# Optimization experiments

Hardware: AMD Instinct MI355X
Metric: run time of the kernel (lower is better)

The kernel has to match this reference:

```python
import jax, jax.numpy as jnp
import numpy as np

B, C, H, W = 1, 512, 64, 64
HEADS, DIM_HEAD = 8, 64
GROUPS = 32
EPS = 1e-5
SCALE = DIM_HEAD ** -0.5


def setup_inputs() -> dict:
    key = jax.random.key(0)
    ks = jax.random.split(key, 8)
    inner = HEADS * DIM_HEAD  # 512
    s = 0.02
    return {
        "hidden_states": jax.random.normal(ks[0], (B, C, H, W), jnp.float32),
        "gn_gamma": jnp.ones((C,), jnp.float32),
        "gn_beta": jnp.zeros((C,), jnp.float32),
        "wq": jax.random.normal(ks[1], (inner, C), jnp.float32) * s,
        "wk": jax.random.normal(ks[2], (inner, C), jnp.float32) * s,
        "wv": jax.random.normal(ks[3], (inner, C), jnp.float32) * s,
        "wo": jax.random.normal(ks[4], (C, inner), jnp.float32) * s,
        "bo": jnp.zeros((C,), jnp.float32),
    }


def _group_norm(x, gamma, beta):
    # x: [B, C, H, W]; normalize within channel groups over (C//G, H, W)
    b, c, h, w = x.shape
    xg = x.reshape(b, GROUPS, c // GROUPS, h, w)
    mean = xg.mean(axis=(2, 3, 4), keepdims=True)
    var = xg.var(axis=(2, 3, 4), keepdims=True)
    xg = (xg - mean) * jax.lax.rsqrt(var + EPS)
    x = xg.reshape(b, c, h, w)
    return x * gamma[None, :, None, None] + beta[None, :, None, None]


def reference(hidden_states, gn_gamma, gn_beta, wq, wk, wv, wo, bo):
    residual = hidden_states
    x = _group_norm(hidden_states, gn_gamma, gn_beta)
    b, c, h, w = x.shape
    n = h * w
    x = x.reshape(b, c, n).transpose(0, 2, 1)  # [B, N, C]

    # torch Linear: y = x @ W^T (bias=False for q/k/v)
    q = (x @ wq.T).reshape(b, n, HEADS, DIM_HEAD).transpose(0, 2, 1, 3)  # [B,H,N,D]
    k = (x @ wk.T).reshape(b, n, HEADS, DIM_HEAD).transpose(0, 2, 1, 3)
    v = (x @ wv.T).reshape(b, n, HEADS, DIM_HEAD).transpose(0, 2, 1, 3)

    scores = jnp.einsum("bhqd,bhkd->bhqk", q, k) * SCALE  # [B,H,N,N]
    probs = jax.nn.softmax(scores, axis=-1)
    out = jnp.einsum("bhqk,bhkd->bhqd", probs, v)  # [B,H,N,D]

    out = out.transpose(0, 2, 1, 3).reshape(b, n, HEADS * DIM_HEAD)  # [B,N,inner]
    out = out @ wo.T + bo  # [B,N,C]
    out = out.transpose(0, 2, 1).reshape(b, c, h, w)
    return out + residual
```

## Files before the change

kernel.cpp:

```cpp
#include <hip/hip_runtime.h>

#define N_TOK 4096
#define C_DIM 512
#define NH    8
#define EPS   1e-5f
#define NSPLIT 4
#define THR   11.0f

typedef __attribute__((ext_vector_type(8))) __bf16 bf16x8;
typedef __attribute__((ext_vector_type(4))) float  f32x4;
using u16 = unsigned short;
using u32 = unsigned int;

#define MFMA16 __builtin_amdgcn_mfma_f32_16x16x32_bf16

__device__ __forceinline__ u16 f2bf(float f){
  u32 x = __builtin_bit_cast(u32, f);
  x += 0x7fffu + ((x>>16)&1u);
  return (u16)(x>>16);
}
__device__ __forceinline__ float bf2f(u16 v){
  return __builtin_bit_cast(float, (u32)v<<16);
}
__device__ __forceinline__ float exp2a(float x){
  float r; asm("v_exp_f32 %0, %1" : "=v"(r) : "v"(x)); return r;
}
__device__ __forceinline__ u32 cvtpk(float lo, float hi){
  u32 r; asm("v_cvt_pk_bf16_f32 %0, %1, %2" : "=v"(r) : "v"(lo), "v"(hi)); return r;
}
__device__ __forceinline__ float max3a(float a, float b, float c){
  float r; asm("v_max3_f32 %0, %1, %2, %3" : "=v"(r) : "v"(a), "v"(b), "v"(c)); return r;
}
__device__ __forceinline__ void dma16(const void* src, void* lds){
  __builtin_amdgcn_global_load_lds(
      (const __attribute__((address_space(1))) u32*)src,
      (__attribute__((address_space(3))) u32*)lds, 16, 0, 0);
}

__global__ __launch_bounds__(256) void k_pre(const float* __restrict__ s0,
      const float* __restrict__ s1, const float* __restrict__ s2,
      const float* __restrict__ s3, u16* __restrict__ d0, u16* __restrict__ d1,
      u16* __restrict__ d2, u16* __restrict__ d3,
      const float* __restrict__ x, float* __restrict__ pstat,
      u16* __restrict__ xbf){
  __shared__ float rs[4], rss[4];
  int b = blockIdx.x;
  if (b < 1024){
    int m = b >> 8;
    int i = (b & 255)*256 + threadIdx.x;
    const float* s = m==0?s0 : m==1?s1 : m==2?s2 : s3;
    u16*         d = m==0?d0 : m==1?d1 : m==2?d2 : d3;
    float4 v = ((const float4*)s)[i];
    ushort4 o; o.x=f2bf(v.x); o.y=f2bf(v.y); o.z=f2bf(v.z); o.w=f2bf(v.w);
    ((ushort4*)d)[i] = o;
    return;
  }
  int gb = b - 1024;
  int g = gb>>3, p = gb&7, t = threadIdx.x;
  const float4* gx4 = (const float4*)(x + (size_t)g*16*N_TOK) + (size_t)p*2048;
  ushort4* xb4 = (ushort4*)xbf + (size_t)g*16384 + (size_t)p*2048;
  float s=0.f, ss=0.f;
  #pragma unroll
  for (int k=0;k<8;k++){
    float4 v = gx4[t + k*256];
    s  += v.x+v.y+v.z+v.w;
    ss += v.x*v.x+v.y*v.y+v.z*v.z+v.w*v.w;
    ushort4 o; o.x=f2bf(v.x); o.y=f2bf(v.y); o.z=f2bf(v.z); o.w=f2bf(v.w);
    xb4[t + k*256] = o;
  }
  for (int m=1;m<64;m<<=1){ s += __shfl_xor(s,m); ss += __shfl_xor(ss,m); }
  int w=t>>6, lane=t&63;
  if (lane==0){ rs[w]=s; rss[w]=ss; }
  __syncthreads();
  if (t==0){
    pstat[(g*8+p)*2  ] = rs[0]+rs[1]+rs[2]+rs[3];
    pstat[(g*8+p)*2+1] = rss[0]+rss[1]+rss[2]+rss[3];
  }
}

__global__ __launch_bounds__(256) void k_gn_apply(const u16* __restrict__ xbf,
      const float* __restrict__ pstat, const float* __restrict__ gamma,
      const float* __restrict__ beta, u16* __restrict__ X){
  int g = blockIdx.x, c0 = g*16;
  int n = blockIdx.y*256 + threadIdx.x;
  float S=0.f, SS=0.f;
  #pragma unroll
  for (int p=0;p<8;p++){ S += pstat[(g*8+p)*2]; SS += pstat[(g*8+p)*2+1]; }
  float mean = S*(1.f/65536.f);
  float rstd = rsqrtf(SS*(1.f/65536.f) - mean*mean + EPS);
  u16 ov[16];
  #pragma unroll
  for (int c=0;c<16;c++){
    float gm = gamma[c0+c]*rstd;
    float be = beta[c0+c] - mean*gm;
    float v  = bf2f(xbf[(size_t)(c0+c)*N_TOK + n])*gm + be;
    ov[c] = f2bf(v);
  }
  uint4* dst = (uint4*)&X[(size_t)n*C_DIM + c0];
  dst[0] = *(uint4*)&ov[0];
  dst[1] = *(uint4*)&ov[8];
}

__device__ __forceinline__ void gemm_core64(const u16* A, const u16* B,
      int m0, int n0, char* LDS, f32x4 (&acc)[4][2]){
  int t = threadIdx.x, w = t>>6, l = t&63, lr = l&15, li = l>>4;
  int wr = w>>1, wc = w&1;
  char* As = LDS;
  char* Bs = LDS + 32768;
  const char* Ac = (const char*)A + (size_t)m0*1024;
  const char* Bc = (const char*)B + (size_t)n0*1024;
  int rswz = (lr&7)<<4;

  int rowA[4], segA[4], rowB[2], segB[2];
  #pragma unroll
  for (int k=0;k<4;k++){ int s=t+k*256; rowA[k]=s>>3; segA[k]=s&7; }
  #pragma unroll
  for (int k=0;k<2;k++){ int s=t+k*256; rowB[k]=s>>3; segB[k]=s&7; }

  #define STAGE(it, bb) { int koff=(it)*128;                                   \
    _Pragma("unroll")                                                          \
    for (int k=0;k<4;k++){                                                     \
      int ys = (segA[k]*16) ^ ((rowA[k]&7)<<4);                                \
      dma16(Ac + (size_t)rowA[k]*1024 + koff + ys,                             \
            As + (bb)*16384 + w*1024 + k*4096);                                \
    }                                                                          \
    _Pragma("unroll")                                                          \
    for (int k=0;k<2;k++){                                                     \
      int ys = (segB[k]*16) ^ ((rowB[k]&7)<<4);                                \
      dma16(Bc + (size_t)rowB[k]*1024 + koff + ys,                             \
            Bs + (bb)*8192 + w*1024 + k*4096);                                 \
    } }

  STAGE(0, 0);
  __syncthreads();

  int buf = 0;
  for (int it=0; it<8; it++){
    if (it < 7){ STAGE(it+1, buf^1); }
    char* Ab = As + buf*16384;
    char* Bb = Bs + buf*8192;
    #pragma unroll
    for (int ks=0; ks<2; ks++){
      bf16x8 af[4], bfr[2];
      #pragma unroll
      for (int i=0;i<4;i++){
        int ra = wr*64 + i*16 + lr;
        af[i]  = *(const bf16x8*)(Ab + ra*128 + ((li*16 + ks*64) ^ rswz));
      }
      #pragma unroll
      for (int j=0;j<2;j++){
        int rb = wc*32 + j*16 + lr;
        bfr[j] = *(const bf16x8*)(Bb + rb*128 + ((li*16 + ks*64) ^ rswz));
      }
      __builtin_amdgcn_s_setprio(1);
      #pragma unroll
      for (int i=0;i<4;i++){
        #pragma unroll
        for (int j=0;j<2;j++){
          acc[i][j] = MFMA16(af[i], bfr[j], acc[i][j], 0,0,0);
        }
      }
      __builtin_amdgcn_s_setprio(0);
    }
    __syncthreads();
    buf ^= 1;
  }
  #undef STAGE
}

__global__ __launch_bounds__(256,3) void k_qkv2(const u16* __restrict__ X,
      const u16* __restrict__ wq, const u16* __restrict__ wk,
      const u16* __restrict__ wv, u16* __restrict__ Qo, u16* __restrict__ Ko,
      u16* __restrict__ Vto){
  __shared__ char LDS[49152];
  int b = blockIdx.x;
  const u16 *A, *B; u16* Cp; int ldc, m0, n0; float sc = 1.f; bool vperm = false;
  if (b < 256){        A=X;  B=wq; Cp=Qo;  ldc=512;  m0=(b>>3)*128; n0=(b&7)*64;
                       sc = 0.125f*1.44269504f; }
  else if (b < 512){ int r=b-256; A=X;  B=wk; Cp=Ko;  ldc=512;  m0=(r>>3)*128; n0=(r&7)*64; }
  else             { int r=b-512; A=wv; B=X;  Cp=Vto; ldc=4096; m0=(r>>6)*128; n0=(r&63)*64;
                     vperm = true; }

  f32x4 acc[4][2] = {};
  gemm_core64(A, B, m0, n0, LDS, acc);

  int t = threadIdx.x, w = t>>6, l = t&63, lr = l&15, li = l>>4;
  int wr = w>>1, wc = w&1;
  #pragma unroll
  for (int i=0;i<4;i++){
    #pragma unroll
    for (int rr=0;rr<4;rr++){
      int mm = m0 + wr*64 + i*16 + li*4 + rr;
      #pragma unroll
      for (int j=0;j<2;j++){
        int nn = n0 + wc*32 + j*16 + lr;
        if (vperm){
          int tl = nn & 63;
          int pos = (tl & 35) | ((tl & 12) << 1) | ((tl & 16) >> 2);
          nn = (nn & ~63) | pos;
        }
        Cp[(size_t)mm*ldc + nn] = f2bf(acc[i][j][rr]*sc);
      }
    }
  }
}

__global__ __launch_bounds__(256,3) void k_oproj2(const u16* __restrict__ Wo,
      const u16* __restrict__ Ob, const float* __restrict__ bo,
      const float* __restrict__ res, float* __restrict__ out){
  __shared__ char LDS[49152];
  int b = blockIdx.x;
  int m0 = (b>>6)*128, n0 = (b&63)*64;

  f32x4 acc[4][2] = {};
  gemm_core64(Wo, Ob, m0, n0, LDS, acc);

  int t = threadIdx.x, w = t>>6, l = t&63, lr = l&15, li = l>>4;
  int wr = w>>1, wc = w&1;
  #pragma unroll
  for (int i=0;i<4;i++){
    #pragma unroll
    for (int rr=0;rr<4;rr++){
      int cc = m0 + wr*64 + i*16 + li*4 + rr;
      float bias = bo[cc];
      #pragma unroll
      for (int j=0;j<2;j++){
        int nn = n0 + wc*32 + j*16 + lr;
        size_t off = (size_t)cc*4096 + nn;
        out[off] = acc[i][j][rr] + bias + res[off];
      }
    }
  }
}

__global__ __launch_bounds__(256,4) void k_attn6(const u16* __restrict__ Q,
      const u16* __restrict__ K, const u16* __restrict__ Vt,
      u16* __restrict__ Opart, float* __restrict__ ml){
  __shared__ char KV[2][16384];
  int h = blockIdx.y, sp = blockIdx.z;
  int q0 = blockIdx.x*128;
  int t = threadIdx.x, w = t>>6, l = t&63, lr = l&15, li = l>>4;
  char* KVb = (char*)KV;
  int qbase = q0 + w*32;

  const u16* Qp = Q + (size_t)(qbase + lr)*512 + h*64 + li*8;
  bf16x8 qa00 = *(const bf16x8*)(Qp);
  bf16x8 qa01 = *(const bf16x8*)(Qp + 32);
  bf16x8 qa10 = *(const bf16x8*)(Qp + 16*512);
  bf16x8 qa11 = *(const bf16x8*)(Qp + 16*512 + 32);

  int srow = l>>3, y0 = (l&7)*16;
  const char* Kc = (const char*)K;
  const char* Vc = (const char*)Vt;
  const char* ksrc[2]; const char* vsrc[2]; int ldso[2];
  #pragma unroll
  for (int j=0;j<2;j++){
    int row = w*16 + j*8 + srow;
    int ys  = y0 ^ ((row&7)<<4);
    ksrc[j] = Kc + (size_t)(sp*1024 + row)*1024 + h*128 + ys;
    vsrc[j] = Vc + (size_t)(h*64 + row)*8192 + sp*2048 + ys;
    ldso[j] = w*2048 + j*1024;
  }

  #pragma unroll
  for (int j=0;j<2;j++){
    dma16(ksrc[j], KVb + ldso[j]);
    dma16(vsrc[j], KVb + 8192 + ldso[j]);
  }
  __syncthreads();

  f32x4 acc0[4] = {}; f32x4 acc1[4] = {};
  float m0=-1e30f, m1=-1e30f, l0=0.f, l1=0.f;
  int buf = 0;

  for (int it=0; it<16; it++){
    if (it < 15){
      int nb = buf^1;
      #pragma unroll
      for (int j=0;j<2;j++){
        dma16(ksrc[j] + (size_t)(it+1)*65536, KVb + nb*16384 + ldso[j]);
        dma16(vsrc[j] + (it+1)*128,           KVb + nb*16384 + 8192 + ldso[j]);
      }
    }
    char* Klb = KVb + buf*16384;
    char* Vlb = Klb + 8192;

    f32x4 st0[4] = {}; f32x4 st1[4] = {};
    __builtin_amdgcn_s_setprio(1);
    #pragma unroll
    for (int T=0;T<4;T++){
      int row = T*16 + lr, swz = (row&7)<<4;
      const char* rb = Klb + row*128;
      bf16x8 k0 = *(const bf16x8*)(rb + ((li*16     ) ^ swz));
      bf16x8 k1 = *(const bf16x8*)(rb + ((li*16 + 64) ^ swz));
      st0[T] = MFMA16(k0, qa00, st0[T], 0,0,0);
      st0[T] = MFMA16(k1, qa01, st0[T], 0,0,0);
      st1[T] = MFMA16(k0, qa10, st1[T], 0,0,0);
      st1[T] = MFMA16(k1, qa11, st1[T], 0,0,0);
    }
    __builtin_amdgcn_s_setprio(0);

    u32 pk0[8], pk1[8];
    {
      float a0 = max3a(st0[0][0],st0[0][1],st0[0][2]);
      float a1 = max3a(st0[1][0],st0[1][1],st0[1][2]);
      float a2 = max3a(st0[2][0],st0[2][1],st0[2][2]);
      float a3 = max3a(st0[3][0],st0[3][1],st0[3][2]);
      float b0 = max3a(st0[0][3],st0[1][3],st0[2][3]);
      float pmax = fmaxf(max3a(a0,a1,a2), max3a(a3,b0,st0[3][3]));
      pmax = fmaxf(pmax, __shfl_xor(pmax,16));
      pmax = fmaxf(pmax, __shfl_xor(pmax,32));
      if (!__all(pmax <= m0 + THR)){
        float mnew = fmaxf(m0, pmax);
        float fac = exp2a(m0 - mnew);
        m0 = mnew; l0 *= fac;
        float f0=__shfl(fac, li*20+0), f1=__shfl(fac, li*20+1);
        float f2=__shfl(fac, li*20+2), f3=__shfl(fac, li*20+3);
        #pragma unroll
        for (int T=0;T<4;T++){
          acc0[T][0]*=f0; acc0[T][1]*=f1; acc0[T][2]*=f2; acc0[T][3]*=f3;
        }
      }
      float lad = 0.f;
      #pragma unroll
      for (int T=0;T<4;T++){
        float p0=exp2a(st0[T][0]-m0), p1=exp2a(st0[T][1]-m0);
        float p2=exp2a(st0[T][2]-m0), p3=exp2a(st0[T][3]-m0);
        lad += (p0+p1)+(p2+p3);
        pk0[T*2]   = cvtpk(p0,p1);
        pk0[T*2+1] = cvtpk(p2,p3);
      }
      l0 += lad;
    }
    {
      float a0 = max3a(st1[0][0],st1[0][1],st1[0][2]);
      float a1 = max3a(st1[1][0],st1[1][1],st1[1][2]);
      float a2 = max3a(st1[2][0],st1[2][1],st1[2][2]);
      float a3 = max3a(st1[3][0],st1[3][1],st1[3][2]);
      float b0 = max3a(st1[0][3],st1[1][3],st1[2][3]);
      float pmax = fmaxf(max3a(a0,a1,a2), max3a(a3,b0,st1[3][3]));
      pmax = fmaxf(pmax, __shfl_xor(pmax,16));
      pmax = fmaxf(pmax, __shfl_xor(pmax,32));
      if (!__all(pmax <= m1 + THR)){
        float mnew = fmaxf(m1, pmax);
        float fac = exp2a(m1 - mnew);
        m1 = mnew; l1 *= fac;
        float f0=__shfl(fac, li*20+0), f1=__shfl(fac, li*20+1);
        float f2=__shfl(fac, li*20+2), f3=__shfl(fac, li*20+3);
        #pragma unroll
        for (int T=0;T<4;T++){
          acc1[T][0]*=f0; acc1[T][1]*=f1; acc1[T][2]*=f2; acc1[T][3]*=f3;
        }
      }
      float lad = 0.f;
      #pragma unroll
      for (int T=0;T<4;T++){
        float p0=exp2a(st1[T][0]-m1), p1=exp2a(st1[T][1]-m1);
        float p2=exp2a(st1[T][2]-m1), p3=exp2a(st1[T][3]-m1);
        lad += (p0+p1)+(p2+p3);
        pk1[T*2]   = cvtpk(p0,p1);
        pk1[T*2+1] = cvtpk(p2,p3);
      }
      l1 += lad;
    }

    __builtin_amdgcn_s_setprio(1);
    #pragma unroll
    for (int c=0;c<2;c++){
      union { bf16x8 v; u32 u[4]; } A0, A1;
      #pragma unroll
      for (int k=0;k<4;k++){ A0.u[k]=pk0[c*4+k]; A1.u[k]=pk1[c*4+k]; }
      #pragma unroll
      for (int T=0;T<4;T++){
        int vrow = T*16 + lr, vswz = (vrow&7)<<4;
        bf16x8 vb = *(const bf16x8*)(Vlb + vrow*128 + ((c*64 + li*16) ^ vswz));
        acc0[T] = MFMA16(A0.v, vb, acc0[T], 0,0,0);
        acc1[T] = MFMA16(A1.v, vb, acc1[T], 0,0,0);
      }
    }
    __builtin_amdgcn_s_setprio(0);

    __syncthreads();
    buf ^= 1;
  }

  l0 += __shfl_xor(l0,16); l0 += __shfl_xor(l0,32);
  l1 += __shfl_xor(l1,16); l1 += __shfl_xor(l1,32);
  u16* Op = Opart + (size_t)sp*N_TOK*C_DIM;
  #pragma unroll
  for (int T=0;T<4;T++){
    #pragma unroll
    for (int r=0;r<4;r++){
      Op[(size_t)(qbase      + li*4 + r)*512 + h*64 + T*16 + lr] = f2bf(acc0[T][r]);
      Op[(size_t)(qbase + 16 + li*4 + r)*512 + h*64 + T*16 + lr] = f2bf(acc1[T][r]);
    }
  }
  if (li==0){
    float* p0 = ml + (((size_t)sp*NH + h)*N_TOK + qbase + lr)*2;
    p0[0]=m0; p0[1]=l0;
    float* p1 = ml + (((size_t)sp*NH + h)*N_TOK + qbase + 16 + lr)*2;
    p1[0]=m1; p1[1]=l1;
  }
}

__global__ __launch_bounds__(256) void k_merge2(const u16* __restrict__ Opart,
      const float* __restrict__ ml, u16* __restrict__ Ob){
  int i  = blockIdx.x*256 + threadIdx.x;
  int q  = i >> 7;
  int c4 = i & 127;
  int h  = c4 >> 4;
  float m[NSPLIT], lv[NSPLIT];
  #pragma unroll
  for (int s=0;s<NSPLIT;s++){
    const float* p = ml + (((size_t)s*NH + h)*N_TOK + q)*2;
    m[s]=p[0]; lv[s]=p[1];
  }
  float M = fmaxf(max3a(m[0],m[1],m[2]), m[3]);
  float wgt[NSPLIT]; float L = 0.f;
  #pragma unroll
  for (int s=0;s<NSPLIT;s++){ wgt[s] = exp2a(m[s]-M); L += lv[s]*wgt[s]; }
  float inv = 1.f/L;
  float4 o = {0.f,0.f,0.f,0.f};
  #pragma unroll
  for (int s=0;s<NSPLIT;s++){
    ushort4 a = ((const ushort4*)(Opart + (size_t)s*N_TOK*C_DIM))[i];
    o.x += bf2f(a.x)*wgt[s]; o.y += bf2f(a.y)*wgt[s];
    o.z += bf2f(a.z)*wgt[s]; o.w += bf2f(a.w)*wgt[s];
  }
  ushort4 r;
  r.x=f2bf(o.x*inv); r.y=f2bf(o.y*inv); r.z=f2bf(o.z*inv); r.w=f2bf(o.w*inv);
  ((ushort4*)Ob)[i] = r;
}

extern "C" void kernel_launch(void* const* d_in, const int* in_sizes, int n_in,
                              void* d_out, int out_size, void* d_ws, size_t ws_size,
                              hipStream_t stream){
  (void)in_sizes; (void)n_in; (void)out_size; (void)ws_size;
  const float* hs    = (const float*)d_in[0];
  const float* gamma = (const float*)d_in[1];
  const float* beta  = (const float*)d_in[2];
  const float* wq    = (const float*)d_in[3];
  const float* wk    = (const float*)d_in[4];
  const float* wv    = (const float*)d_in[5];
  const float* wo    = (const float*)d_in[6];
  const float* bo    = (const float*)d_in[7];
  float* out = (float*)d_out;

  u16* X   = (u16*)d_ws;
  u16* Qb  = X   + (size_t)4096*512;
  u16* Kb  = Qb  + (size_t)4096*512;
  u16* Vtb = Kb  + (size_t)4096*512;
  u16* Ob  = Vtb + (size_t)4096*512;
  u16* xbf = Ob  + (size_t)4096*512;
  u16* wqb = xbf + (size_t)4096*512;
  u16* wkb = wqb + (size_t)512*512;
  u16* wvb = wkb + (size_t)512*512;
  u16* wob = wvb + (size_t)512*512;
  float* pstat = (float*)(wob + (size_t)512*512);
  u16* Opart   = (u16*)(pstat + 1024);
  float* mlbuf = (float*)(Opart + (size_t)NSPLIT*4096*512);

  k_pre<<<1280,256,0,stream>>>(wq, wk, wv, wo, wqb, wkb, wvb, wob, hs, pstat, xbf);
  dim3 ga(32, 16);
  k_gn_apply<<<ga,256,0,stream>>>(xbf, pstat, gamma, beta, X);
  k_qkv2<<<768,256,0,stream>>>(X, wqb, wkb, wvb, Qb, Kb, Vtb);
  dim3 gat(32, 8, NSPLIT);
  k_attn6<<<gat,256,0,stream>>>(Qb, Kb, Vtb, Opart, mlbuf);
  k_merge2<<<2048,256,0,stream>>>(Opart, mlbuf, Ob);
  k_oproj2<<<256,256,0,stream>>>(wob, Ob, bo, hs, out);
}
```

Measured before the change: 85.17 us.

## Fuse split-KV merge into output projection and compute row sums via MFMA

Removes the separate merge kernel: the output-projection GEMM now loads the four split partial outputs plus their max/sum stats, combines them in registers and writes the merged bf16 tile into LDS as its B operand. This drops one launch and a full round trip of the merged O buffer through global memory. The attention kernel now accumulates softmax row sums with an extra MFMA against a ones vector instead of VALU adds, and prefetches the first V fragments before the softmax. The o-proj kernel does more per-block work with occupancy lowered to 2, and its global B loads are not async, so they may stall the pipeline. Each o-proj block also redoes the merge arithmetic and stat loads for its own tiles.

New measurement: 98.56 us. 15.7% more time.

```diff
diff --git a/kernel.cpp b/kernel.cpp
--- a/kernel.cpp
+++ b/kernel.cpp
@@ -205,23 +205,123 @@
   }
 }
 
-__global__ __launch_bounds__(256,3) void k_oproj2(const u16* __restrict__ Wo,
-      const u16* __restrict__ Ob, const float* __restrict__ bo,
-      const float* __restrict__ res, float* __restrict__ out){
+__global__ __launch_bounds__(256,2) void k_oproj3(const u16* __restrict__ Wo,
+      const u16* __restrict__ Opart, const float* __restrict__ ml,
+      const float* __restrict__ bo, const float* __restrict__ res,
+      float* __restrict__ out){
   __shared__ char LDS[49152];
   int b = blockIdx.x;
-  int m0 = (b>>6)*128, n0 = (b&63)*64;
-
-  f32x4 acc[4][2] = {};
-  gemm_core64(Wo, Ob, m0, n0, LDS, acc);
-
+  int cm0 = (b>>6)*128, n0 = (b&63)*64;
   int t = threadIdx.x, w = t>>6, l = t&63, lr = l&15, li = l>>4;
   int wr = w>>1, wc = w&1;
+  char* As = LDS;
+  char* Bs = LDS + 32768;
+  const char* Ac = (const char*)Wo + (size_t)cm0*1024;
+  int rswz = (lr&7)<<4;
+
+  int rowA[4], segA[4];
+  #pragma unroll
+  for (int k=0;k<4;k++){ int s=t+k*256; rowA[k]=s>>3; segA[k]=s&7; }
+  int tok[2]; size_t bofs[2];
+  #pragma unroll
+  for (int k=0;k<2;k++){
+    int s=t+k*256; int row=s>>3; int seg=s&7;
+    tok[k] = n0 + row;
+    bofs[k] = (size_t)tok[k]*1024 + ((seg*16) ^ ((row&7)<<4));
+  }
+
+  #define ASTAGE(it, bb) { int koff=(it)*128;                                  \
+    _Pragma("unroll")                                                          \
+    for (int k=0;k<4;k++){                                                     \
+      int ys = (segA[k]*16) ^ ((rowA[k]&7)<<4);                                \
+      dma16(Ac + (size_t)rowA[k]*1024 + koff + ys,                             \
+            As + (bb)*16384 + w*1024 + k*4096);                                \
+    } }
+
+  uint4 pb[2][4];
+  #define BLOAD(hd) {                                                          \
+    _Pragma("unroll")                                                          \
+    for (int k=0;k<2;k++){                                                     \
+      _Pragma("unroll")                                                        \
+      for (int s=0;s<4;s++){                                                   \
+        pb[k][s] = *(const uint4*)((const char*)Opart                          \
+                   + (size_t)s*N_TOK*C_DIM*2 + bofs[k] + (size_t)(hd)*128);    \
+      } } }
+
+  #define BMERGE(hd, bb) {                                                     \
+    _Pragma("unroll")                                                          \
+    for (int k=0;k<2;k++){                                                     \
+      float mm_[4], ll_[4];                                                    \
+      _Pragma("unroll")                                                        \
+      for (int s=0;s<4;s++){                                                   \
+        const float* pp = ml + (((size_t)s*NH + (hd))*N_TOK + tok[k])*2;       \
+        mm_[s]=pp[0]; ll_[s]=pp[1];                                            \
+      }                                                                        \
+      float M = fmaxf(max3a(mm_[0],mm_[1],mm_[2]), mm_[3]);                    \
+      float wg[4]; float L=0.f;                                                \
+      _Pragma("unroll")                                                        \
+      for (int s=0;s<4;s++){ wg[s]=exp2a(mm_[s]-M); L += ll_[s]*wg[s]; }       \
+      float inv = 1.f/L;                                                       \
+      u16 ob[8];                                                               \
+      const u16* e0=(const u16*)&pb[k][0]; const u16* e1=(const u16*)&pb[k][1];\
+      const u16* e2=(const u16*)&pb[k][2]; const u16* e3=(const u16*)&pb[k][3];\
+      _Pragma("unroll")                                                        \
+      for (int j=0;j<8;j++){                                                   \
+        float v = bf2f(e0[j])*wg[0] + bf2f(e1[j])*wg[1]                        \
+                + bf2f(e2[j])*wg[2] + bf2f(e3[j])*wg[3];                       \
+        ob[j] = f2bf(v*inv);                                                   \
+      }                                                                        \
+      *(uint4*)(Bs + (bb)*8192 + w*1024 + k*4096 + l*16) = *(uint4*)ob;        \
+    } }
+
+  f32x4 acc[4][2] = {};
+
+  ASTAGE(0, 0);
+  BLOAD(0);
+  BMERGE(0, 0);
+  __syncthreads();
+
+  int buf = 0;
+  for (int it=0; it<8; it++){
+    if (it < 7){ ASTAGE(it+1, buf^1); BLOAD(it+1); }
+    char* Ab = As + buf*16384;
+    char* Bb = Bs + buf*8192;
+    #pragma unroll
+    for (int ks=0; ks<2; ks++){
+      bf16x8 af[4], bfr[2];
+      #pragma unroll
+      for (int i=0;i<4;i++){
+        int ra = wr*64 + i*16 + lr;
+        af[i]  = *(const bf16x8*)(Ab + ra*128 + ((li*16 + ks*64) ^ rswz));
+      }
+      #pragma unroll
+      for (int j=0;j<2;j++){
+        int rb = wc*32 + j*16 + lr;
+        bfr[j] = *(const bf16x8*)(Bb + rb*128 + ((li*16 + ks*64) ^ rswz));
+      }
+      __builtin_amdgcn_s_setprio(1);
+      #pragma unroll
+      for (int i=0;i<4;i++){
+        #pragma unroll
+        for (int j=0;j<2;j++){
+          acc[i][j] = MFMA16(af[i], bfr[j], acc[i][j], 0,0,0);
+        }
+      }
+      __builtin_amdgcn_s_setprio(0);
+    }
+    if (it < 7){ BMERGE(it+1, buf^1); }
+    __syncthreads();
+    buf ^= 1;
+  }
+  #undef ASTAGE
+  #undef BLOAD
+  #undef BMERGE
+
   #pragma unroll
   for (int i=0;i<4;i++){
     #pragma unroll
     for (int rr=0;rr<4;rr++){
-      int cc = m0 + wr*64 + i*16 + li*4 + rr;
+      int cc = cm0 + wr*64 + i*16 + li*4 + rr;
       float bias = bo[cc];
       #pragma unroll
       for (int j=0;j<2;j++){
@@ -233,7 +333,7 @@
   }
 }
 
-__global__ __launch_bounds__(256,4) void k_attn6(const u16* __restrict__ Q,
+__global__ __launch_bounds__(256,4) void k_attn7(const u16* __restrict__ Q,
       const u16* __restrict__ K, const u16* __restrict__ Vt,
       u16* __restrict__ Opart, float* __restrict__ ml){
   __shared__ char KV[2][16384];
@@ -270,7 +370,11 @@
   __syncthreads();
 
   f32x4 acc0[4] = {}; f32x4 acc1[4] = {};
-  float m0=-1e30f, m1=-1e30f, l0=0.f, l1=0.f;
+  f32x4 lacc0 = {0.f,0.f,0.f,0.f}, lacc1 = {0.f,0.f,0.f,0.f};
+  float m0=-1e30f, m1=-1e30f;
+  union { bf16x8 v; u32 u[4]; } ONES;
+  #pragma unroll
+  for (int k=0;k<4;k++) ONES.u[k] = 0x3F803F80u;
   int buf = 0;
 
   for (int it=0; it<16; it++){
@@ -299,6 +403,13 @@
       st1[T] = MFMA16(k1, qa11, st1[T], 0,0,0);
     }
     __builtin_amdgcn_s_setprio(0);
+
+    bf16x8 vf0[4];
+    #pragma unroll
+    for (int T=0;T<4;T++){
+      int vrow = T*16 + lr, vswz = (vrow&7)<<4;
+      vf0[T] = *(const bf16x8*)(Vlb + vrow*128 + ((li*16) ^ vswz));
+    }
 
     u32 pk0[8], pk1[8];
     {
@@ -313,24 +424,22 @@
       if (!__all(pmax <= m0 + THR)){
         float mnew = fmaxf(m0, pmax);
         float fac = exp2a(m0 - mnew);
-        m0 = mnew; l0 *= fac;
+        m0 = mnew;
         float f0=__shfl(fac, li*20+0), f1=__shfl(fac, li*20+1);
         float f2=__shfl(fac, li*20+2), f3=__shfl(fac, li*20+3);
         #pragma unroll
         for (int T=0;T<4;T++){
           acc0[T][0]*=f0; acc0[T][1]*=f1; acc0[T][2]*=f2; acc0[T][3]*=f3;
         }
-      }
-      float lad = 0.f;
+        lacc0[0]*=f0; lacc0[1]*=f1; lacc0[2]*=f2; lacc0[3]*=f3;
+      }
       #pragma unroll
       for (int T=0;T<4;T++){
         float p0=exp2a(st0[T][0]-m0), p1=exp2a(st0[T][1]-m0);
         float p2=exp2a(st0[T][2]-m0), p3=exp2a(st0[T][3]-m0);
-        lad += (p0+p1)+(p2+p3);
         pk0[T*2]   = cvtpk(p0,p1);
         pk0[T*2+1] = cvtpk(p2,p3);
       }
-      l0 += lad;
     }
     {
       float a0 = max3a(st1[0][0],st1[0][1],st1[0][2]);
@@ -344,24 +453,22 @@
       if (!__all(pmax <= m1 + THR)){
         float mnew = fmaxf(m1, pmax);
         float fac = exp2a(m1 - mnew);
-        m1 = mnew; l1 *= fac;
+        m1 = mnew;
         float f0=__shfl(fac, li*20+0), f1=__shfl(fac, li*20+1);
         float f2=__shfl(fac, li*20+2), f3=__shfl(fac, li*20+3);
         #pragma unroll
         for (int T=0;T<4;T++){
           acc1[T][0]*=f0; acc1[T][1]*=f1; acc1[T][2]*=f2; acc1[T][3]*=f3;
         }
-      }
-      float lad = 0.f;
+        lacc1[0]*=f0; lacc1[1]*=f1; lacc1[2]*=f2; lacc1[3]*=f3;
+      }
       #pragma unroll
       for (int T=0;T<4;T++){
         float p0=exp2a(st1[T][0]-m1), p1=exp2a(st1[T][1]-m1);
         float p2=exp2a(st1[T][2]-m1), p3=exp2a(st1[T][3]-m1);
-        lad += (p0+p1)+(p2+p3);
         pk1[T*2]   = cvtpk(p0,p1);
         pk1[T*2+1] = cvtpk(p2,p3);
       }
-      l1 += lad;
     }
 
     __builtin_amdgcn_s_setprio(1);
@@ -372,11 +479,17 @@
       for (int k=0;k<4;k++){ A0.u[k]=pk0[c*4+k]; A1.u[k]=pk1[c*4+k]; }
       #pragma unroll
       for (int T=0;T<4;T++){
-        int vrow = T*16 + lr, vswz = (vrow&7)<<4;
-        bf16x8 vb = *(const bf16x8*)(Vlb + vrow*128 + ((c*64 + li*16) ^ vswz));
+        bf16x8 vb;
+        if (c==0) vb = vf0[T];
+        else {
+          int vrow = T*16 + lr, vswz = (vrow&7)<<4;
+          vb = *(const bf16x8*)(Vlb + vrow*128 + ((64 + li*16) ^ vswz));
+        }
         acc0[T] = MFMA16(A0.v, vb, acc0[T], 0,0,0);
         acc1[T] = MFMA16(A1.v, vb, acc1[T], 0,0,0);
       }
+      lacc0 = MFMA16(A0.v, ONES.v, lacc0, 0,0,0);
+      lacc1 = MFMA16(A1.v, ONES.v, lacc1, 0,0,0);
     }
     __builtin_amdgcn_s_setprio(0);
 
@@ -384,8 +497,12 @@
     buf ^= 1;
   }
 
-  l0 += __shfl_xor(l0,16); l0 += __shfl_xor(l0,32);
-  l1 += __shfl_xor(l1,16); l1 += __shfl_xor(l1,32);
+  float mq0[4], mq1[4];
+  #pragma unroll
+  for (int r=0;r<4;r++){
+    mq0[r] = __shfl(m0, li*4+r);
+    mq1[r] = __shfl(m1, li*4+r);
+  }
   u16* Op = Opart + (size_t)sp*N_TOK*C_DIM;
   #pragma unroll
   for (int T=0;T<4;T++){
@@ -395,41 +512,15 @@
       Op[(size_t)(qbase + 16 + li*4 + r)*512 + h*64 + T*16 + lr] = f2bf(acc1[T][r]);
     }
   }
-  if (li==0){
-    float* p0 = ml + (((size_t)sp*NH + h)*N_TOK + qbase + lr)*2;
-    p0[0]=m0; p0[1]=l0;
-    float* p1 = ml + (((size_t)sp*NH + h)*N_TOK + qbase + 16 + lr)*2;
-    p1[0]=m1; p1[1]=l1;
-  }
-}
-
-__global__ __launch_bounds__(256) void k_merge2(const u16* __restrict__ Opart,
-      const float* __restrict__ ml, u16* __restrict__ Ob){
-  int i  = blockIdx.x*256 + threadIdx.x;
-  int q  = i >> 7;
-  int c4 = i & 127;
-  int h  = c4 >> 4;
-  float m[NSPLIT], lv[NSPLIT];
-  #pragma unroll
-  for (int s=0;s<NSPLIT;s++){
-    const float* p = ml + (((size_t)s*NH + h)*N_TOK + q)*2;
-    m[s]=p[0]; lv[s]=p[1];
-  }
-  float M = fmaxf(max3a(m[0],m[1],m[2]), m[3]);
-  float wgt[NSPLIT]; float L = 0.f;
-  #pragma unroll
-  for (int s=0;s<NSPLIT;s++){ wgt[s] = exp2a(m[s]-M); L += lv[s]*wgt[s]; }
-  float inv = 1.f/L;
-  float4 o = {0.f,0.f,0.f,0.f};
-  #pragma unroll
-  for (int s=0;s<NSPLIT;s++){
-    ushort4 a = ((const ushort4*)(Opart + (size_t)s*N_TOK*C_DIM))[i];
-    o.x += bf2f(a.x)*wgt[s]; o.y += bf2f(a.y)*wgt[s];
-    o.z += bf2f(a.z)*wgt[s]; o.w += bf2f(a.w)*wgt[s];
-  }
-  ushort4 r;
-  r.x=f2bf(o.x*inv); r.y=f2bf(o.y*inv); r.z=f2bf(o.z*inv); r.w=f2bf(o.w*inv);
-  ((ushort4*)Ob)[i] = r;
+  if (lr==0){
+    #pragma unroll
+    for (int r=0;r<4;r++){
+      float* p0 = ml + (((size_t)sp*NH + h)*N_TOK + qbase + li*4 + r)*2;
+      p0[0]=mq0[r]; p0[1]=lacc0[r];
+      float* p1 = ml + (((size_t)sp*NH + h)*N_TOK + qbase + 16 + li*4 + r)*2;
+      p1[0]=mq1[r]; p1[1]=lacc1[r];
+    }
+  }
 }
 
 extern "C" void kernel_launch(void* const* d_in, const int* in_sizes, int n_in,
@@ -450,8 +541,7 @@
   u16* Qb  = X   + (size_t)4096*512;
   u16* Kb  = Qb  + (size_t)4096*512;
   u16* Vtb = Kb  + (size_t)4096*512;
-  u16* Ob  = Vtb + (size_t)4096*512;
-  u16* xbf = Ob  + (size_t)4096*512;
+  u16* xbf = Vtb + (size_t)4096*512;
   u16* wqb = xbf + (size_t)4096*512;
   u16* wkb = wqb + (size_t)512*512;
   u16* wvb = wkb + (size_t)512*512;
@@ -465,7 +555,6 @@
   k_gn_apply<<<ga,256,0,stream>>>(xbf, pstat, gamma, beta, X);
   k_qkv2<<<768,256,0,stream>>>(X, wqb, wkb, wvb, Qb, Kb, Vtb);
   dim3 gat(32, 8, NSPLIT);
-  k_attn6<<<gat,256,0,stream>>>(Qb, Kb, Vtb, Opart, mlbuf);
-  k_merge2<<<2048,256,0,stream>>>(Opart, mlbuf, Ob);
-  k_oproj2<<<256,256,0,stream>>>(wob, Ob, bo, hs, out);
-}
+  k_attn7<<<gat,256,0,stream>>>(Qb, Kb, Vtb, Opart, mlbuf);
+  k_oproj3<<<256,256,0,stream>>>(wob, Opart, mlbuf, bo, hs, out);
+}
```
